# Kernel tuning notes

Measured on AMD Instinct MI355X. Metric: run time of the kernel, lower is better.

## Reference

```python
import jax, jax.numpy as jnp
import numpy as np

N = 8192
D_IN = 256
D_OUT = 256
E = 131072
P = 2  # number of bottom-to-up hierarchy levels


def gcn_conv(x, edge_index, W, b, num_nodes):
    """PyG-style GCNConv: add self-loops, symmetric normalization, x @ W + b."""
    loops = jnp.arange(num_nodes)
    src = jnp.concatenate([edge_index[0], loops])
    dst = jnp.concatenate([edge_index[1], loops])
    deg = jax.ops.segment_sum(jnp.ones_like(dst, dtype=x.dtype), dst,
                              num_segments=num_nodes)  # [N], >=1 due to self-loops
    dinv = jax.lax.rsqrt(deg)
    norm = dinv[src] * dinv[dst]                         # [E+N]
    h = x @ W                                            # [N, out]
    out = jax.ops.segment_sum(norm[:, None] * h[src], dst, num_segments=num_nodes)
    return out + b


def setup_inputs() -> dict:
    key = jax.random.key(0)
    ks = jax.random.split(key, 8)
    embedding = jax.random.normal(ks[0], (N, D_IN), dtype=jnp.float32)
    down2up_path = jax.random.uniform(ks[1], (P, N, N), dtype=jnp.float32)
    same_level_edge_index = jax.random.randint(ks[2], (2, E), 0, N)
    up2down_edge_index = jax.random.randint(ks[3], (2, E), 0, N)
    W_same = jax.random.normal(ks[4], (D_IN, D_OUT), dtype=jnp.float32) * (1.0 / np.sqrt(D_IN))
    b_same = jnp.zeros((D_OUT,), dtype=jnp.float32)
    W_top = jax.random.normal(ks[5], (D_OUT, D_OUT), dtype=jnp.float32) * (1.0 / np.sqrt(D_OUT))
    b_top = jnp.zeros((D_OUT,), dtype=jnp.float32)
    return {"embedding": embedding, "down2up_path": down2up_path,
            "same_level_edge_index": same_level_edge_index,
            "up2down_edge_index": up2down_edge_index,
            "W_same": W_same, "b_same": b_same,
            "W_top": W_top, "b_top": b_top}


def reference(embedding, down2up_path, same_level_edge_index, up2down_edge_index,
              W_same, b_same, W_top, b_top):
    # ---- bottom_to_up (MEAN path): per-level mm + residual add + row-mean normalize
    emb = embedding
    for p in range(down2up_path.shape[0]):  # small fixed number of hierarchy levels
        A = down2up_path[p]                  # [N, N]
        emb = (emb + A @ emb) * (1.0 / (A.sum(-1) + 1.0))[:, None]
    # ---- same-level GCNConv
    emb = gcn_conv(emb, same_level_edge_index, W_same, b_same, N)
    # ---- top_to_bottom GCNConv
    emb = gcn_conv(emb, up2down_edge_index, W_top, b_top, N)
    return emb
```

## Files before the change

### kernel.cpp

```cpp
#include <hip/hip_runtime.h>
#include <cstdint>

#define NN 8192
#define DD 256
#define KS 4

typedef unsigned short u16;
typedef __bf16 bf16x8 __attribute__((ext_vector_type(8)));
typedef float f32x4 __attribute__((ext_vector_type(4)));

__device__ __forceinline__ u16 f2bf(float f) {
    union { float f; unsigned u; } c; c.f = f;
    unsigned u = c.u;
    return (u16)((u + 0x7FFFu + ((u >> 16) & 1u)) >> 16);
}

template<bool AF32, bool ROWSUM>
__global__ __launch_bounds__(256, 2)
void gemm_k(const void* __restrict__ Ap, long ldA,
            const u16* __restrict__ BT, long ldBT,
            float* __restrict__ C, float* __restrict__ rs, int kPer)
{
    __shared__ __align__(16) u16 As[64 * 32];
    __shared__ __align__(16) u16 Bs[256 * 32];

    const int tid  = threadIdx.x;
    const int lane = tid & 63;
    const int wave = tid >> 6;
    const int r    = lane & 15;
    const int q    = lane >> 4;
    const long m0  = (long)blockIdx.x * 64;
    const long k0  = (long)blockIdx.z * kPer;
    float* __restrict__ Cs = C + (long)blockIdx.z * ((long)NN * DD);

    f32x4 acc[4][4] = {};
    f32x4 racc[4]   = {};
    bf16x8 ones;
    if constexpr (ROWSUM) {
        union { bf16x8 v; u16 u[8]; } cv;
        u16 pat = (r == 0) ? (u16)0x3F80 : (u16)0;
        #pragma unroll
        for (int j = 0; j < 8; ++j) cv.u[j] = pat;
        ones = cv.v;
    }

    const u16* bBase = BT + (long)(wave * 64 + r) * ldBT + k0 + q * 8;
    const int arow = tid >> 2;
    const int kq8  = tid & 3;
    const float* aBaseF = AF32 ? ((const float*)Ap + (m0 + arow) * ldA + k0 + kq8 * 8) : nullptr;
    const u16* aBaseH = AF32 ? nullptr
                             : ((const u16*)Ap + (m0 + wave * 16 + r) * ldA + k0 + q * 8);
    const int nsteps = kPer >> 5;

    for (int s = 0; s < nsteps; ++s) {
        const long koff = (long)s << 5;
        if constexpr (AF32) {
            const float* ap = aBaseF + koff;
            f32x4 f0 = __builtin_nontemporal_load((const f32x4*)ap);
            f32x4 f1 = __builtin_nontemporal_load((const f32x4*)(ap + 4));
            union { u16 u[8]; uint4 v; } pk;
            pk.u[0] = f2bf(f0[0]); pk.u[1] = f2bf(f0[1]);
            pk.u[2] = f2bf(f0[2]); pk.u[3] = f2bf(f0[3]);
            pk.u[4] = f2bf(f1[0]); pk.u[5] = f2bf(f1[1]);
            pk.u[6] = f2bf(f1[2]); pk.u[7] = f2bf(f1[3]);
            *(uint4*)(As + (arow >> 4) * 512 + (kq8 * 16 + (arow & 15)) * 8) = pk.v;
        } else {
            __builtin_amdgcn_global_load_lds(
                (const __attribute__((address_space(1))) void*)(aBaseH + koff),
                (__attribute__((address_space(3))) void*)(As + wave * 512 + lane * 8),
                16, 0, 0);
        }
        #pragma unroll
        for (int g2 = 0; g2 < 4; ++g2) {
            __builtin_amdgcn_global_load_lds(
                (const __attribute__((address_space(1))) void*)(bBase + (long)g2 * 16 * ldBT + koff),
                (__attribute__((address_space(3))) void*)(Bs + (wave * 4 + g2) * 512 + lane * 8),
                16, 0, 0);
        }
        __syncthreads();

        bf16x8 af[4], bfr[4];
        #pragma unroll
        for (int i = 0; i < 4; ++i) {
            af[i]  = *(const bf16x8*)(As + i * 512 + lane * 8);
            bfr[i] = *(const bf16x8*)(Bs + (wave * 4 + i) * 512 + lane * 8);
        }
        #pragma unroll
        for (int i = 0; i < 4; ++i)
            #pragma unroll
            for (int j = 0; j < 4; ++j)
                acc[i][j] = __builtin_amdgcn_mfma_f32_16x16x32_bf16(af[i], bfr[j], acc[i][j], 0, 0, 0);
        if constexpr (ROWSUM) {
            if (wave == 0) {
                #pragma unroll
                for (int i = 0; i < 4; ++i)
                    racc[i] = __builtin_amdgcn_mfma_f32_16x16x32_bf16(af[i], ones, racc[i], 0, 0, 0);
            }
        }
        __syncthreads();
    }

    #pragma unroll
    for (int i = 0; i < 4; ++i) {
        const long rowb = m0 + i * 16 + q * 4;
        #pragma unroll
        for (int j = 0; j < 4; ++j) {
            const long col = wave * 64 + j * 16 + r;
            #pragma unroll
            for (int rr2 = 0; rr2 < 4; ++rr2)
                Cs[(rowb + rr2) * DD + col] = acc[i][j][rr2];
        }
        if constexpr (ROWSUM) {
            if (wave == 0 && r == 0) {
                #pragma unroll
                for (int rr2 = 0; rr2 < 4; ++rr2)
                    rs[(long)blockIdx.z * NN + rowb + rr2] = racc[i][rr2];
            }
        }
    }
}

__global__ __launch_bounds__(256)
void tc_k(const float* __restrict__ src, u16* __restrict__ dst, int R, int C)
{
    __shared__ u16 t[64][72];
    const int tid = threadIdx.x;
    const int rr = tid >> 2;
    const int cc = (tid & 3) << 4;
    const long r0 = (long)blockIdx.x * 64;
    const long c0 = (long)blockIdx.y * 64;
    const float* sp = src + (r0 + rr) * C + c0 + cc;
    #pragma unroll
    for (int j = 0; j < 16; ++j) t[cc + j][rr] = f2bf(sp[j]);
    __syncthreads();
    u16* dp = dst + (c0 + rr) * (long)R + r0 + cc;
    #pragma unroll
    for (int j = 0; j < 16; ++j) dp[j] = t[rr][cc + j];
}

__global__ __launch_bounds__(256)
void norm0_k(const float* __restrict__ Cacc, const float* __restrict__ rs,
             const float* __restrict__ resid,
             float* __restrict__ outF, u16* __restrict__ outT)
{
    __shared__ u16 t[64][72];
    const int tid = threadIdx.x;
    const int rr = tid >> 2;
    const int cc = (tid & 3) << 4;
    const long i0 = (long)blockIdx.x * 64;
    const int  n0 = blockIdx.y * 64;
    const long i  = i0 + rr;
    const float rsum = rs[i] + rs[NN + i] + rs[2 * NN + i] + rs[3 * NN + i];
    const float scale = 1.0f / (rsum + 1.0f);
    const float* c0p = Cacc + i * DD + n0 + cc;
    const float* rp  = resid + i * DD + n0 + cc;
    float* fp = outF + i * DD + n0 + cc;
    const long slab = (long)NN * DD;
    #pragma unroll
    for (int j = 0; j < 16; ++j) {
        float v = rp[j] + c0p[j] + c0p[j + slab] + c0p[j + 2 * slab] + c0p[j + 3 * slab];
        v *= scale;
        fp[j] = v;
        t[cc + j][rr] = f2bf(v);
    }
    __syncthreads();
    u16* op = outT + (long)(n0 + rr) * NN + i0 + cc;
    #pragma unroll
    for (int j = 0; j < 16; ++j) op[j] = t[rr][cc + j];
}

__global__ __launch_bounds__(256)
void norm1_k(const float* __restrict__ Cacc, const float* __restrict__ rs,
             const float* __restrict__ resid, u16* __restrict__ outR)
{
    const long g = ((long)blockIdx.x * 256 + threadIdx.x) * 4;
    const long row = g >> 8;
    const float rsum = rs[row] + rs[NN + row] + rs[2 * NN + row] + rs[3 * NN + row];
    const float scale = 1.0f / (rsum + 1.0f);
    const long slab = (long)NN * DD;
    const float4 c0 = *(const float4*)(Cacc + g);
    const float4 c1 = *(const float4*)(Cacc + g + slab);
    const float4 c2 = *(const float4*)(Cacc + g + 2 * slab);
    const float4 c3 = *(const float4*)(Cacc + g + 3 * slab);
    const float4 rv = *(const float4*)(resid + g);
    u16* op = outR + g;
    op[0] = f2bf((rv.x + c0.x + c1.x + c2.x + c3.x) * scale);
    op[1] = f2bf((rv.y + c0.y + c1.y + c2.y + c3.y) * scale);
    op[2] = f2bf((rv.z + c0.z + c1.z + c2.z + c3.z) * scale);
    op[3] = f2bf((rv.w + c0.w + c1.w + c2.w + c3.w) * scale);
}

__global__ __launch_bounds__(256)
void count_k(const int* __restrict__ dst, int E, int* __restrict__ counts) {
    int e = blockIdx.x * 256 + threadIdx.x;
    if (e < E) atomicAdd(counts + dst[e], 1);
}

__global__ __launch_bounds__(1024)
void scan_k(const int* __restrict__ counts, int* __restrict__ offs,
            int* __restrict__ cursor, float* __restrict__ dinv) {
    __shared__ int wpre[17];
    __shared__ int sbase;
    const int tid  = threadIdx.x;
    const int lane = tid & 63;
    const int wid  = tid >> 6;
    if (tid == 0) { sbase = 0; wpre[0] = 0; }
    __syncthreads();
    for (int base = 0; base < NN; base += 1024) {
        const int c = counts[base + tid];
        dinv[base + tid] = 1.0f / sqrtf((float)c + 1.0f);
        int x = c;
        #pragma unroll
        for (int d = 1; d < 64; d <<= 1) {
            int y = __shfl_up(x, d, 64);
            if (lane >= d) x += y;
        }
        if (lane == 63) wpre[wid + 1] = x;
        __syncthreads();
        if (wid == 0) {
            int w = (lane < 16) ? wpre[lane + 1] : 0;
            #pragma unroll
            for (int d = 1; d < 16; d <<= 1) {
                int y = __shfl_up(w, d, 64);
                if (lane >= d) w += y;
            }
            if (lane < 16) wpre[lane + 1] = w;
        }
        __syncthreads();
        const int excl = sbase + wpre[wid] + (x - c);
        offs[base + tid]   = excl;
        cursor[base + tid] = excl;
        __syncthreads();
        if (tid == 0) sbase += wpre[16];
    }
    if (tid == 0) offs[NN] = sbase;
}

__global__ __launch_bounds__(256)
void fill_k(const int* __restrict__ src, const int* __restrict__ dst, int E,
            int* __restrict__ cursor, int* __restrict__ csr) {
    int e = blockIdx.x * 256 + threadIdx.x;
    if (e < E) {
        int p = atomicAdd(cursor + dst[e], 1);
        csr[p] = src[e];
    }
}

__global__ __launch_bounds__(256)
void gather_k(const float* __restrict__ h,
              const int* __restrict__ offs,
              const int* __restrict__ csr,
              const float* __restrict__ dinv,
              const float* __restrict__ bias,
              u16* __restrict__ outBF,
              float* __restrict__ outF)
{
    const int node = blockIdx.x * 4 + (threadIdx.x >> 6);
    const int lane = threadIdx.x & 63;
    const float di = dinv[node];
    const float4 hs = ((const float4*)(h + (long)node * DD))[lane];
    const float s0 = di * di;
    float4 acc;
    acc.x = hs.x * s0; acc.y = hs.y * s0; acc.z = hs.z * s0; acc.w = hs.w * s0;

    const int b0 = offs[node], b1 = offs[node + 1];
    int e = b0;
    for (; e + 2 <= b1; e += 2) {
        const int sa = csr[e], sb = csr[e + 1];
        const float wa = di * dinv[sa];
        const float wb = di * dinv[sb];
        const float4 xa = ((const float4*)(h + (long)sa * DD))[lane];
        const float4 xb = ((const float4*)(h + (long)sb * DD))[lane];
        acc.x += wa * xa.x + wb * xb.x;
        acc.y += wa * xa.y + wb * xb.y;
        acc.z += wa * xa.z + wb * xb.z;
        acc.w += wa * xa.w + wb * xb.w;
    }
    if (e < b1) {
        const int s = csr[e];
        const float w = di * dinv[s];
        const float4 x = ((const float4*)(h + (long)s * DD))[lane];
        acc.x += w * x.x; acc.y += w * x.y; acc.z += w * x.z; acc.w += w * x.w;
    }
    const float4 bv = ((const float4*)bias)[lane];
    acc.x += bv.x; acc.y += bv.y; acc.z += bv.z; acc.w += bv.w;

    if (outF) {
        ((float4*)(outF + (long)node * DD))[lane] = acc;
    } else {
        u16* op = outBF + (long)node * DD + lane * 4;
        op[0] = f2bf(acc.x); op[1] = f2bf(acc.y);
        op[2] = f2bf(acc.z); op[3] = f2bf(acc.w);
    }
}

extern "C" void kernel_launch(void* const* d_in, const int* in_sizes, int n_in,
                              void* d_out, int out_size, void* d_ws, size_t ws_size,
                              hipStream_t stream)
{
    (void)n_in; (void)out_size; (void)ws_size;
    const float* emb0  = (const float*)d_in[0];
    const float* A     = (const float*)d_in[1];
    const int*   eiS   = (const int*)d_in[2];
    const int*   eiU   = (const int*)d_in[3];
    const float* Wsame = (const float*)d_in[4];
    const float* bsame = (const float*)d_in[5];
    const float* Wtop  = (const float*)d_in[6];
    const float* btop  = (const float*)d_in[7];
    const int E = in_sizes[2] / 2;

    char* ws = (char*)d_ws;
    u16*   embT   = (u16*)  (ws + 0);
    float* Cacc   = (float*)(ws + 4194304);
    float* emb1   = (float*)(ws + 37748736);
    u16*   xbf    = (u16*)  (ws + 46137344);
    u16*   WT     = (u16*)  (ws + 50331648);
    float* rsb    = (float*)(ws + 50462720);
    float* dinv   = (float*)(ws + 50593792);
    int*   counts = (int*)  (ws + 50626560);
    int*   offs   = (int*)  (ws + 50659328);
    int*   cursor = (int*)  (ws + 50696192);
    int*   csr    = (int*)  (ws + 50728960);

    const dim3 blk(256);
    const dim3 gDense(128, 1, KS), gGcn(128, 1, 1);
    const dim3 gE((E + 255) / 256), gG(NN / 4);

    tc_k<<<dim3(128, 4), blk, 0, stream>>>(emb0, embT, NN, DD);

    gemm_k<true, true><<<gDense, blk, 0, stream>>>(A, NN, embT, NN, Cacc, rsb, NN / KS);
    norm0_k<<<dim3(128, 4), blk, 0, stream>>>(Cacc, rsb, emb0, emb1, embT);

    gemm_k<true, true><<<gDense, blk, 0, stream>>>(A + (size_t)NN * NN, NN, embT, NN, Cacc, rsb, NN / KS);
    norm1_k<<<dim3(2048), blk, 0, stream>>>(Cacc, rsb, emb1, xbf);

    tc_k<<<dim3(4, 4), blk, 0, stream>>>(Wsame, WT, DD, DD);
    hipMemsetAsync(counts, 0, 32768, stream);
    count_k<<<gE, blk, 0, stream>>>(eiS + E, E, counts);
    scan_k<<<dim3(1), dim3(1024), 0, stream>>>(counts, offs, cursor, dinv);
    fill_k<<<gE, blk, 0, stream>>>(eiS, eiS + E, E, cursor, csr);
    gemm_k<false, false><<<gGcn, blk, 0, stream>>>(xbf, DD, WT, DD, Cacc, nullptr, 256);
    gather_k<<<gG, blk, 0, stream>>>(Cacc, offs, csr, dinv, bsame, xbf, nullptr);

    tc_k<<<dim3(4, 4), blk, 0, stream>>>(Wtop, WT, DD, DD);
    hipMemsetAsync(counts, 0, 32768, stream);
    count_k<<<gE, blk, 0, stream>>>(eiU + E, E, counts);
    scan_k<<<dim3(1), dim3(1024), 0, stream>>>(counts, offs, cursor, dinv);
    fill_k<<<gE, blk, 0, stream>>>(eiU, eiU + E, E, cursor, csr);
    gemm_k<false, false><<<gGcn, blk, 0, stream>>>(xbf, DD, WT, DD, Cacc, nullptr, 256);
    gather_k<<<gG, blk, 0, stream>>>(Cacc, offs, csr, dinv, btop, nullptr, (float*)d_out);
}
```

Baseline: 991.7 us.

## Double-buffer GEMM LDS tiles, batch both graph CSR builds, shuffle-broadcast gather indices

The GEMM main loop now uses two LDS buffers, issuing the next K-step's global loads before the current MFMA block so load latency can overlap compute. The A conversion store is deferred until after the MFMAs. Both GCN layers' weight transposes, degree counts, scans and CSR fills are merged into single two-way kernels launched once at the start. The gather kernel loads up to 64 neighbor indices and weights per wave cooperatively, then broadcasts them via shuffles with 4-way unrolled row loads. The LDS footprint doubles, which may reduce occupancy for the dense GEMM.

```diff
diff --git a/kernel.cpp b/kernel.cpp
--- a/kernel.cpp
+++ b/kernel.cpp
@@ -13,6 +13,15 @@
     union { float f; unsigned u; } c; c.f = f;
     unsigned u = c.u;
     return (u16)((u + 0x7FFFu + ((u >> 16) & 1u)) >> 16);
+}
+
+__device__ __forceinline__ void cvt_store8(f32x4 a, f32x4 b, u16* dst) {
+    union { u16 u[8]; uint4 v; } pk;
+    pk.u[0] = f2bf(a[0]); pk.u[1] = f2bf(a[1]);
+    pk.u[2] = f2bf(a[2]); pk.u[3] = f2bf(a[3]);
+    pk.u[4] = f2bf(b[0]); pk.u[5] = f2bf(b[1]);
+    pk.u[6] = f2bf(b[2]); pk.u[7] = f2bf(b[3]);
+    *(uint4*)dst = pk.v;
 }
 
 template<bool AF32, bool ROWSUM>
@@ -21,8 +30,8 @@
             const u16* __restrict__ BT, long ldBT,
             float* __restrict__ C, float* __restrict__ rs, int kPer)
 {
-    __shared__ __align__(16) u16 As[64 * 32];
-    __shared__ __align__(16) u16 Bs[256 * 32];
+    __shared__ __align__(16) u16 As[2][64 * 32];
+    __shared__ __align__(16) u16 Bs[2][256 * 32];
 
     const int tid  = threadIdx.x;
     const int lane = tid & 63;
@@ -48,42 +57,57 @@
     const int arow = tid >> 2;
     const int kq8  = tid & 3;
     const float* aBaseF = AF32 ? ((const float*)Ap + (m0 + arow) * ldA + k0 + kq8 * 8) : nullptr;
+    u16* const aDst0 = &As[0][(arow >> 4) * 512 + (kq8 * 16 + (arow & 15)) * 8];
+    u16* const aDst1 = &As[1][(arow >> 4) * 512 + (kq8 * 16 + (arow & 15)) * 8];
     const u16* aBaseH = AF32 ? nullptr
                              : ((const u16*)Ap + (m0 + wave * 16 + r) * ldA + k0 + q * 8);
     const int nsteps = kPer >> 5;
 
-    for (int s = 0; s < nsteps; ++s) {
-        const long koff = (long)s << 5;
-        if constexpr (AF32) {
-            const float* ap = aBaseF + koff;
-            f32x4 f0 = __builtin_nontemporal_load((const f32x4*)ap);
-            f32x4 f1 = __builtin_nontemporal_load((const f32x4*)(ap + 4));
-            union { u16 u[8]; uint4 v; } pk;
-            pk.u[0] = f2bf(f0[0]); pk.u[1] = f2bf(f0[1]);
-            pk.u[2] = f2bf(f0[2]); pk.u[3] = f2bf(f0[3]);
-            pk.u[4] = f2bf(f1[0]); pk.u[5] = f2bf(f1[1]);
-            pk.u[6] = f2bf(f1[2]); pk.u[7] = f2bf(f1[3]);
-            *(uint4*)(As + (arow >> 4) * 512 + (kq8 * 16 + (arow & 15)) * 8) = pk.v;
-        } else {
-            __builtin_amdgcn_global_load_lds(
-                (const __attribute__((address_space(1))) void*)(aBaseH + koff),
-                (__attribute__((address_space(3))) void*)(As + wave * 512 + lane * 8),
-                16, 0, 0);
-        }
-        #pragma unroll
-        for (int g2 = 0; g2 < 4; ++g2) {
-            __builtin_amdgcn_global_load_lds(
-                (const __attribute__((address_space(1))) void*)(bBase + (long)g2 * 16 * ldBT + koff),
-                (__attribute__((address_space(3))) void*)(Bs + (wave * 4 + g2) * 512 + lane * 8),
-                16, 0, 0);
-        }
-        __syncthreads();
-
+#define STAGE_B(t, buf) do {                                                      \
+    const long koff_ = (long)(t) << 5;                                            \
+    _Pragma("unroll")                                                             \
+    for (int g2_ = 0; g2_ < 4; ++g2_)                                             \
+        __builtin_amdgcn_global_load_lds(                                         \
+            (const __attribute__((address_space(1))) void*)(bBase + (long)g2_ * 16 * ldBT + koff_), \
+            (__attribute__((address_space(3))) void*)(&Bs[buf][(wave * 4 + g2_) * 512 + lane * 8]), \
+            16, 0, 0);                                                            \
+  } while (0)
+
+#define STAGE_AH(t, buf)                                                          \
+    __builtin_amdgcn_global_load_lds(                                             \
+        (const __attribute__((address_space(1))) void*)(aBaseH + ((long)(t) << 5)), \
+        (__attribute__((address_space(3))) void*)(&As[buf][wave * 512 + lane * 8]), \
+        16, 0, 0)
+
+    STAGE_B(0, 0);
+    if constexpr (AF32) {
+        f32x4 p0 = __builtin_nontemporal_load((const f32x4*)aBaseF);
+        f32x4 p1 = __builtin_nontemporal_load((const f32x4*)(aBaseF + 4));
+        cvt_store8(p0, p1, aDst0);
+    } else {
+        STAGE_AH(0, 0);
+    }
+    __syncthreads();
+
+    for (int t = 0; t < nsteps; ++t) {
+        const int cur = t & 1, nxt = cur ^ 1;
+        const bool more = (t + 1 < nsteps);
+        f32x4 na0, na1;
+        if (more) {
+            STAGE_B(t + 1, nxt);
+            if constexpr (AF32) {
+                const float* ap = aBaseF + ((long)(t + 1) << 5);
+                na0 = __builtin_nontemporal_load((const f32x4*)ap);
+                na1 = __builtin_nontemporal_load((const f32x4*)(ap + 4));
+            } else {
+                STAGE_AH(t + 1, nxt);
+            }
+        }
         bf16x8 af[4], bfr[4];
         #pragma unroll
         for (int i = 0; i < 4; ++i) {
-            af[i]  = *(const bf16x8*)(As + i * 512 + lane * 8);
-            bfr[i] = *(const bf16x8*)(Bs + (wave * 4 + i) * 512 + lane * 8);
+            af[i]  = *(const bf16x8*)(&As[cur][i * 512 + lane * 8]);
+            bfr[i] = *(const bf16x8*)(&Bs[cur][(wave * 4 + i) * 512 + lane * 8]);
         }
         #pragma unroll
         for (int i = 0; i < 4; ++i)
@@ -97,8 +121,13 @@
                     racc[i] = __builtin_amdgcn_mfma_f32_16x16x32_bf16(af[i], ones, racc[i], 0, 0, 0);
             }
         }
+        if constexpr (AF32) {
+            if (more) cvt_store8(na0, na1, (nxt ? aDst1 : aDst0));
+        }
         __syncthreads();
     }
+#undef STAGE_B
+#undef STAGE_AH
 
     #pragma unroll
     for (int i = 0; i < 4; ++i) {
@@ -134,6 +163,27 @@
     for (int j = 0; j < 16; ++j) t[cc + j][rr] = f2bf(sp[j]);
     __syncthreads();
     u16* dp = dst + (c0 + rr) * (long)R + r0 + cc;
+    #pragma unroll
+    for (int j = 0; j < 16; ++j) dp[j] = t[rr][cc + j];
+}
+
+__global__ __launch_bounds__(256)
+void tcw_k(const float* __restrict__ w0, const float* __restrict__ w1,
+           u16* __restrict__ dst)
+{
+    __shared__ u16 t[64][72];
+    const float* src = blockIdx.z ? w1 : w0;
+    u16* d = dst + (size_t)blockIdx.z * DD * DD;
+    const int tid = threadIdx.x;
+    const int rr = tid >> 2;
+    const int cc = (tid & 3) << 4;
+    const long r0 = (long)blockIdx.x * 64;
+    const long c0 = (long)blockIdx.y * 64;
+    const float* sp = src + (r0 + rr) * DD + c0 + cc;
+    #pragma unroll
+    for (int j = 0; j < 16; ++j) t[cc + j][rr] = f2bf(sp[j]);
+    __syncthreads();
+    u16* dp = d + (c0 + rr) * (long)DD + r0 + cc;
     #pragma unroll
     for (int j = 0; j < 16; ++j) dp[j] = t[rr][cc + j];
 }
@@ -191,14 +241,22 @@
 }
 
 __global__ __launch_bounds__(256)
-void count_k(const int* __restrict__ dst, int E, int* __restrict__ counts) {
-    int e = blockIdx.x * 256 + threadIdx.x;
-    if (e < E) atomicAdd(counts + dst[e], 1);
+void count2_k(const int* __restrict__ dS, const int* __restrict__ dU, int E,
+              int* __restrict__ counts) {
+    const int e = blockIdx.x * 256 + threadIdx.x;
+    const int* d = blockIdx.y ? dU : dS;
+    if (e < E) atomicAdd(counts + blockIdx.y * NN + d[e], 1);
 }
 
 __global__ __launch_bounds__(1024)
-void scan_k(const int* __restrict__ counts, int* __restrict__ offs,
-            int* __restrict__ cursor, float* __restrict__ dinv) {
+void scan2_k(const int* __restrict__ counts, int* __restrict__ offs,
+             int* __restrict__ cursor, float* __restrict__ dinv) {
+    const int p = blockIdx.x;
+    const int* cnt = counts + p * NN;
+    int* off   = offs + p * (NN + 1);
+    int* curp  = cursor + p * NN;
+    float* dv  = dinv + p * NN;
+
     __shared__ int wpre[17];
     __shared__ int sbase;
     const int tid  = threadIdx.x;
@@ -207,8 +265,8 @@
     if (tid == 0) { sbase = 0; wpre[0] = 0; }
     __syncthreads();
     for (int base = 0; base < NN; base += 1024) {
-        const int c = counts[base + tid];
-        dinv[base + tid] = 1.0f / sqrtf((float)c + 1.0f);
+        const int c = cnt[base + tid];
+        dv[base + tid] = 1.0f / sqrtf((float)c + 1.0f);
         int x = c;
         #pragma unroll
         for (int d = 1; d < 64; d <<= 1) {
@@ -227,22 +285,26 @@
             if (lane < 16) wpre[lane + 1] = w;
         }
         __syncthreads();
+        const int tot  = wpre[16];
         const int excl = sbase + wpre[wid] + (x - c);
-        offs[base + tid]   = excl;
-        cursor[base + tid] = excl;
+        off[base + tid]  = excl;
+        curp[base + tid] = excl;
         __syncthreads();
-        if (tid == 0) sbase += wpre[16];
-    }
-    if (tid == 0) offs[NN] = sbase;
-}
-
-__global__ __launch_bounds__(256)
-void fill_k(const int* __restrict__ src, const int* __restrict__ dst, int E,
-            int* __restrict__ cursor, int* __restrict__ csr) {
-    int e = blockIdx.x * 256 + threadIdx.x;
+        if (tid == 0) sbase += tot;
+    }
+    if (tid == 0) off[NN] = sbase;
+}
+
+__global__ __launch_bounds__(256)
+void fill2_k(const int* __restrict__ eiS, const int* __restrict__ eiU, int E,
+             int* __restrict__ cursor, int* __restrict__ csr) {
+    const int e = blockIdx.x * 256 + threadIdx.x;
+    const int p = blockIdx.y;
+    const int* src = p ? eiU : eiS;
+    const int* dst = src + E;
     if (e < E) {
-        int p = atomicAdd(cursor + dst[e], 1);
-        csr[p] = src[e];
+        int pos = atomicAdd(cursor + p * NN + dst[e], 1);
+        csr[p * ((1 << 17) + NN) + pos] = src[e];
     }
 }
 
@@ -264,23 +326,35 @@
     acc.x = hs.x * s0; acc.y = hs.y * s0; acc.z = hs.z * s0; acc.w = hs.w * s0;
 
     const int b0 = offs[node], b1 = offs[node + 1];
-    int e = b0;
-    for (; e + 2 <= b1; e += 2) {
-        const int sa = csr[e], sb = csr[e + 1];
-        const float wa = di * dinv[sa];
-        const float wb = di * dinv[sb];
-        const float4 xa = ((const float4*)(h + (long)sa * DD))[lane];
-        const float4 xb = ((const float4*)(h + (long)sb * DD))[lane];
-        acc.x += wa * xa.x + wb * xb.x;
-        acc.y += wa * xa.y + wb * xb.y;
-        acc.z += wa * xa.z + wb * xb.z;
-        acc.w += wa * xa.w + wb * xb.w;
-    }
-    if (e < b1) {
-        const int s = csr[e];
-        const float w = di * dinv[s];
-        const float4 x = ((const float4*)(h + (long)s * DD))[lane];
-        acc.x += w * x.x; acc.y += w * x.y; acc.z += w * x.z; acc.w += w * x.w;
+    for (int base = b0; base < b1; base += 64) {
+        const int nb = (b1 - base < 64) ? (b1 - base) : 64;
+        int   sidx = node;
+        float wv   = 0.0f;
+        if (lane < nb) {
+            sidx = csr[base + lane];
+            wv   = di * dinv[sidx];
+        }
+        int e = 0;
+        for (; e + 4 <= nb; e += 4) {
+            const int   i0 = __shfl(sidx, e),     i1 = __shfl(sidx, e + 1);
+            const int   i2 = __shfl(sidx, e + 2), i3 = __shfl(sidx, e + 3);
+            const float w0 = __shfl(wv, e),       w1 = __shfl(wv, e + 1);
+            const float w2 = __shfl(wv, e + 2),   w3 = __shfl(wv, e + 3);
+            const float4 x0 = ((const float4*)(h + (long)i0 * DD))[lane];
+            const float4 x1 = ((const float4*)(h + (long)i1 * DD))[lane];
+            const float4 x2 = ((const float4*)(h + (long)i2 * DD))[lane];
+            const float4 x3 = ((const float4*)(h + (long)i3 * DD))[lane];
+            acc.x += w0 * x0.x + w1 * x1.x + w2 * x2.x + w3 * x3.x;
+            acc.y += w0 * x0.y + w1 * x1.y + w2 * x2.y + w3 * x3.y;
+            acc.z += w0 * x0.z + w1 * x1.z + w2 * x2.z + w3 * x3.z;
+            acc.w += w0 * x0.w + w1 * x1.w + w2 * x2.w + w3 * x3.w;
+        }
+        for (; e < nb; ++e) {
+            const int   s = __shfl(sidx, e);
+            const float w = __shfl(wv, e);
+            const float4 x = ((const float4*)(h + (long)s * DD))[lane];
+            acc.x += w * x.x; acc.y += w * x.y; acc.z += w * x.z; acc.w += w * x.w;
+        }
     }
     const float4 bv = ((const float4*)bias)[lane];
     acc.x += bv.x; acc.y += bv.y; acc.z += bv.z; acc.w += bv.w;
@@ -308,6 +382,7 @@
     const float* Wtop  = (const float*)d_in[6];
     const float* btop  = (const float*)d_in[7];
     const int E = in_sizes[2] / 2;
+    const int CSRSZ = (1 << 17) + NN;
 
     char* ws = (char*)d_ws;
     u16*   embT   = (u16*)  (ws + 0);
@@ -315,18 +390,23 @@
     float* emb1   = (float*)(ws + 37748736);
     u16*   xbf    = (u16*)  (ws + 46137344);
     u16*   WT     = (u16*)  (ws + 50331648);
-    float* rsb    = (float*)(ws + 50462720);
-    float* dinv   = (float*)(ws + 50593792);
-    int*   counts = (int*)  (ws + 50626560);
-    int*   offs   = (int*)  (ws + 50659328);
-    int*   cursor = (int*)  (ws + 50696192);
-    int*   csr    = (int*)  (ws + 50728960);
+    float* rsb    = (float*)(ws + 50593792);
+    float* dinv2  = (float*)(ws + 50724864);
+    int*   counts = (int*)  (ws + 50790400);
+    int*   offs2  = (int*)  (ws + 50855936);
+    int*   cursor = (int*)  (ws + 50921488);
+    int*   csr2   = (int*)  (ws + 50987024);
 
     const dim3 blk(256);
     const dim3 gDense(128, 1, KS), gGcn(128, 1, 1);
-    const dim3 gE((E + 255) / 256), gG(NN / 4);
+    const dim3 gE2((E + 255) / 256, 2), gG(NN / 4);
 
     tc_k<<<dim3(128, 4), blk, 0, stream>>>(emb0, embT, NN, DD);
+    tcw_k<<<dim3(4, 4, 2), blk, 0, stream>>>(Wsame, Wtop, WT);
+    hipMemsetAsync(counts, 0, 65536, stream);
+    count2_k<<<gE2, blk, 0, stream>>>(eiS + E, eiU + E, E, counts);
+    scan2_k<<<dim3(2), dim3(1024), 0, stream>>>(counts, offs2, cursor, dinv2);
+    fill2_k<<<gE2, blk, 0, stream>>>(eiS, eiU, E, cursor, csr2);
 
     gemm_k<true, true><<<gDense, blk, 0, stream>>>(A, NN, embT, NN, Cacc, rsb, NN / KS);
     norm0_k<<<dim3(128, 4), blk, 0, stream>>>(Cacc, rsb, emb0, emb1, embT);
@@ -334,19 +414,10 @@
     gemm_k<true, true><<<gDense, blk, 0, stream>>>(A + (size_t)NN * NN, NN, embT, NN, Cacc, rsb, NN / KS);
     norm1_k<<<dim3(2048), blk, 0, stream>>>(Cacc, rsb, emb1, xbf);
 
-    tc_k<<<dim3(4, 4), blk, 0, stream>>>(Wsame, WT, DD, DD);
-    hipMemsetAsync(counts, 0, 32768, stream);
-    count_k<<<gE, blk, 0, stream>>>(eiS + E, E, counts);
-    scan_k<<<dim3(1), dim3(1024), 0, stream>>>(counts, offs, cursor, dinv);
-    fill_k<<<gE, blk, 0, stream>>>(eiS, eiS + E, E, cursor, csr);
     gemm_k<false, false><<<gGcn, blk, 0, stream>>>(xbf, DD, WT, DD, Cacc, nullptr, 256);
-    gather_k<<<gG, blk, 0, stream>>>(Cacc, offs, csr, dinv, bsame, xbf, nullptr);
-
-    tc_k<<<dim3(4, 4), blk, 0, stream>>>(Wtop, WT, DD, DD);
-    hipMemsetAsync(counts, 0, 32768, stream);
-    count_k<<<gE, blk, 0, stream>>>(eiU + E, E, counts);
-    scan_k<<<dim3(1), dim3(1024), 0, stream>>>(counts, offs, cursor, dinv);
-    fill_k<<<gE, blk, 0, stream>>>(eiU, eiU + E, E, cursor, csr);
-    gemm_k<false, false><<<gGcn, blk, 0, stream>>>(xbf, DD, WT, DD, Cacc, nullptr, 256);
-    gather_k<<<gG, blk, 0, stream>>>(Cacc, offs, csr, dinv, btop, nullptr, (float*)d_out);
-}
+    gather_k<<<gG, blk, 0, stream>>>(Cacc, offs2, csr2, dinv2, bsame, xbf, nullptr);
+
+    gemm_k<false, false><<<gGcn, blk, 0, stream>>>(xbf, DD, WT + DD * DD, DD, Cacc, nullptr, 256);
+    gather_k<<<gG, blk, 0, stream>>>(Cacc, offs2 + (NN + 1), csr2 + CSRSZ,
+                                     dinv2 + NN, btop, nullptr, (float*)d_out);
+}
```

After: 925.5 us. -6.7%, faster.
